# Kernel tuning notes

Hardware: AMD Instinct MI355X
Metric: run time of the kernel (lower is better)

The kernel has to match this reference:

```python
import jax, jax.numpy as jnp
import numpy as np

N = 100000
E = 1600000
IN_CH, HID_CH, OUT_CH, HEADS = 128, 32, 64, 4
NEG_SLOPE = 0.2


def gat_conv(x, src, dst, W, att_src, att_dst, bias, concat):
    """PyG-style GATConv (inference; dropout off). src/dst include self-loops.
    x: [N, Fin], W: [Fin, H*C], att_*: [H, C], bias: [H*C] or [C]."""
    n = x.shape[0]
    H, C = att_src.shape
    h = (x @ W).reshape(n, H, C)                      # [N, H, C]
    a_s = jnp.sum(h * att_src, axis=-1)               # [N, H]
    a_d = jnp.sum(h * att_dst, axis=-1)               # [N, H]
    e = jax.nn.leaky_relu(a_s[src] + a_d[dst], NEG_SLOPE)   # [E, H]
    # segment softmax over incoming edges of each dst node
    e_max = jax.ops.segment_max(e, dst, num_segments=n)     # [N, H]
    e_exp = jnp.exp(e - e_max[dst])                          # [E, H]
    denom = jax.ops.segment_sum(e_exp, dst, num_segments=n) # [N, H]
    alpha = e_exp / (denom[dst] + 1e-16)                     # [E, H]
    msg = h[src] * alpha[:, :, None]                         # [E, H, C]
    out = jax.ops.segment_sum(msg, dst, num_segments=n)     # [N, H, C]
    out = out.reshape(n, H * C) if concat else out.mean(axis=1)
    return out + bias


def setup_inputs() -> dict:
    key = jax.random.key(0)
    ks = jax.random.split(key, 10)
    g = 1.0 / np.sqrt(IN_CH)
    g2 = 1.0 / np.sqrt(HID_CH * HEADS)
    return {
        "x": jax.random.normal(ks[0], (N, IN_CH), dtype=jnp.float32),
        "edge_index": jax.random.randint(ks[1], (2, E), 0, N, dtype=jnp.int64),
        "W1": jax.random.normal(ks[2], (IN_CH, HEADS * HID_CH), dtype=jnp.float32) * g,
        "att_src1": jax.random.normal(ks[3], (HEADS, HID_CH), dtype=jnp.float32) * g,
        "att_dst1": jax.random.normal(ks[4], (HEADS, HID_CH), dtype=jnp.float32) * g,
        "b1": jnp.zeros((HEADS * HID_CH,), dtype=jnp.float32),
        "W2": jax.random.normal(ks[5], (HEADS * HID_CH, OUT_CH), dtype=jnp.float32) * g2,
        "att_src2": jax.random.normal(ks[6], (1, OUT_CH), dtype=jnp.float32) * g2,
        "att_dst2": jax.random.normal(ks[7], (1, OUT_CH), dtype=jnp.float32) * g2,
        "b2": jnp.zeros((OUT_CH,), dtype=jnp.float32),
    }


def reference(x, edge_index, W1, att_src1, att_dst1, b1, W2, att_src2, att_dst2, b2):
    n = x.shape[0]
    # GATConv adds self-loops by default (fixed-size concat: jit friendly)
    loops = jnp.arange(n, dtype=edge_index.dtype)
    src = jnp.concatenate([edge_index[0], loops])
    dst = jnp.concatenate([edge_index[1], loops])
    h = gat_conv(x, src, dst, W1, att_src1, att_dst1, b1, concat=True)
    h = jax.nn.elu(h)
    return gat_conv(h, src, dst, W2, att_src2, att_dst2, b2, concat=False)
```

## Files before the change

kernel.cpp:

```cpp
#include <hip/hip_runtime.h>
#include <hip/hip_fp16.h>

#define NEG_SLOPE 0.2f
#define BKN 128
#define MAXNB 1024
#define GRP 256

typedef _Float16 half_t;
typedef __attribute__((ext_vector_type(4))) _Float16 half4;
typedef __attribute__((ext_vector_type(8))) _Float16 half8;
typedef __attribute__((ext_vector_type(4))) float floatx4;

__device__ __forceinline__ float4 h4_to_f4(half4 h) {
    return make_float4((float)h[0], (float)h[1], (float)h[2], (float)h[3]);
}

__global__ __launch_bounds__(256) void w_convert2(
    const float* __restrict__ W1, half_t* __restrict__ Wt1,
    const float* __restrict__ W2, half_t* __restrict__ Wt2)
{
    int i = blockIdx.x * 256 + threadIdx.x;
    if (i < 128 * 128) {
        int k = i / 128, nn = i % 128;
        Wt1[nn * 128 + k] = (half_t)W1[i];
    } else if (i < 128 * 128 + 128 * 64) {
        int j = i - 128 * 128;
        int k = j / 64, nn = j % 64;
        Wt2[nn * 128 + k] = (half_t)W2[j];
    }
}

template<int BN, int HEADS>
__global__ __launch_bounds__(256) void gemm_mfma(
    const float* __restrict__ X, const half_t* __restrict__ Wt,
    const float* __restrict__ atts, const float* __restrict__ attd,
    half_t* __restrict__ H, float* __restrict__ As, float* __restrict__ Ad,
    int n)
{
    constexpr int K  = 128;
    constexpr int NT = BN / 16;
    constexpr int TPH = NT / HEADS;

    __shared__ half_t Wl[BN * K];
    __shared__ half_t Xl[64 * K];

    const int t = threadIdx.x;
    const int wave = t >> 6, lane = t & 63;
    const int quad = lane >> 4, c = lane & 15;

    float att_s[NT], att_d[NT];
    #pragma unroll
    for (int nt = 0; nt < NT; ++nt) {
        att_s[nt] = atts[nt * 16 + c];
        att_d[nt] = attd[nt * 16 + c];
    }

    for (int i = t; i < BN * 16; i += 256) {
        int row = i >> 4, cid = i & 15;
        half8 v = *(const half8*)(Wt + row * K + cid * 8);
        *(half8*)(Wl + row * K + ((cid ^ (row & 15)) << 3)) = v;
    }

    const int numTiles = (n + 63) / 64;
    for (int tile = blockIdx.x; tile < numTiles; tile += gridDim.x) {
        const int row0 = tile * 64;
        __syncthreads();
        for (int i = t; i < 1024; i += 256) {
            int m = i >> 4, cid = i & 15;
            int row = row0 + m;
            float4 a = make_float4(0.f,0.f,0.f,0.f), b = a;
            if (row < n) {
                const float4* src = (const float4*)(X + (size_t)row * K + cid * 8);
                a = src[0]; b = src[1];
            }
            half8 h;
            h[0]=(half_t)a.x; h[1]=(half_t)a.y; h[2]=(half_t)a.z; h[3]=(half_t)a.w;
            h[4]=(half_t)b.x; h[5]=(half_t)b.y; h[6]=(half_t)b.z; h[7]=(half_t)b.w;
            *(half8*)(Xl + m * K + ((cid ^ (m & 15)) << 3)) = h;
        }
        __syncthreads();

        floatx4 acc[NT];
        #pragma unroll
        for (int i = 0; i < NT; ++i) acc[i] = (floatx4)(0.f);

        #pragma unroll
        for (int kc = 0; kc < 4; ++kc) {
            int cid = kc * 4 + quad;
            half8 afrag = *(const half8*)(Xl + (wave * 16 + c) * K + ((cid ^ c) << 3));
            #pragma unroll
            for (int nt = 0; nt < NT; ++nt) {
                half8 bfrag = *(const half8*)(Wl + (nt * 16 + c) * K + ((cid ^ c) << 3));
                acc[nt] = __builtin_amdgcn_mfma_f32_16x16x32_f16(afrag, bfrag, acc[nt], 0, 0, 0);
            }
        }

        #pragma unroll
        for (int reg = 0; reg < 4; ++reg) {
            int row = row0 + wave * 16 + quad * 4 + reg;
            bool ok = row < n;
            if (ok) {
                #pragma unroll
                for (int nt = 0; nt < NT; ++nt)
                    H[(size_t)row * BN + nt * 16 + c] = (half_t)acc[nt][reg];
            }
            #pragma unroll
            for (int h = 0; h < HEADS; ++h) {
                float ps = 0.f, pd = 0.f;
                #pragma unroll
                for (int u = 0; u < TPH; ++u) {
                    int nt = h * TPH + u;
                    ps += acc[nt][reg] * att_s[nt];
                    pd += acc[nt][reg] * att_d[nt];
                }
                #pragma unroll
                for (int off = 1; off < 16; off <<= 1) {
                    ps += __shfl_xor(ps, off);
                    pd += __shfl_xor(pd, off);
                }
                if (ok && c == 0) {
                    As[(size_t)row * HEADS + h] = ps;
                    Ad[(size_t)row * HEADS + h] = pd;
                }
            }
        }
    }
}

__global__ __launch_bounds__(256) void ghist(
    const int* __restrict__ ei, int E, int Etot, int NB, int chunk,
    int* __restrict__ cnt)
{
    __shared__ int h[MAXNB];
    int g = blockIdx.x;
    for (int i = threadIdx.x; i < NB; i += 256) h[i] = 0;
    __syncthreads();
    int lo = g * chunk, hi = min(Etot, lo + chunk);
    for (int e = lo + threadIdx.x; e < hi; e += 256) {
        int dst = (e < E) ? ei[E + e] : (e - E);
        atomicAdd(&h[dst >> 7], 1);
    }
    __syncthreads();
    for (int i = threadIdx.x; i < NB; i += 256) cnt[i * GRP + g] = h[i];
}

__global__ __launch_bounds__(256) void scan_blocks(
    int* __restrict__ data, int n, int* __restrict__ bsum)
{
    __shared__ int s[256];
    int t = threadIdx.x;
    int idx = blockIdx.x * 1024 + t * 4;
    int4 v = make_int4(0, 0, 0, 0);
    if (idx + 3 < n)      v = *(const int4*)(data + idx);
    else {
        if (idx     < n) v.x = data[idx];
        if (idx + 1 < n) v.y = data[idx+1];
        if (idx + 2 < n) v.z = data[idx+2];
        if (idx + 3 < n) v.w = data[idx+3];
    }
    int tsum = v.x + v.y + v.z + v.w;
    s[t] = tsum;
    __syncthreads();
    for (int off = 1; off < 256; off <<= 1) {
        int x = (t >= off) ? s[t - off] : 0;
        __syncthreads();
        s[t] += x;
        __syncthreads();
    }
    int excl = s[t] - tsum;
    if (t == 255) bsum[blockIdx.x] = s[255];
    if (idx     < n) data[idx]     = excl;
    if (idx + 1 < n) data[idx + 1] = excl + v.x;
    if (idx + 2 < n) data[idx + 2] = excl + v.x + v.y;
    if (idx + 3 < n) data[idx + 3] = excl + v.x + v.y + v.z;
}

__global__ __launch_bounds__(256) void scan_sums(int* __restrict__ bsum, int nb)
{
    __shared__ int s[256];
    int t = threadIdx.x;
    int v = (t < nb) ? bsum[t] : 0;
    s[t] = v;
    __syncthreads();
    for (int off = 1; off < 256; off <<= 1) {
        int x = (t >= off) ? s[t - off] : 0;
        __syncthreads();
        s[t] += x;
        __syncthreads();
    }
    if (t < nb) bsum[t] = s[t] - v;
}

__global__ __launch_bounds__(256) void scan_add(
    int* __restrict__ data, int n, const int* __restrict__ bsum)
{
    int i = blockIdx.x * 256 + threadIdx.x;
    if (i < n) data[i] += bsum[i >> 10];
}

__global__ __launch_bounds__(256) void pass1_scatter(
    const int* __restrict__ ei, int E, int Etot, int NB, int chunk,
    const int* __restrict__ S, unsigned* __restrict__ tmp)
{
    __shared__ int cur[MAXNB];
    int g = blockIdx.x;
    for (int i = threadIdx.x; i < NB; i += 256) cur[i] = S[i * GRP + g];
    __syncthreads();
    int lo = g * chunk, hi = min(Etot, lo + chunk);
    for (int e = lo + threadIdx.x; e < hi; e += 256) {
        int src, dst;
        if (e < E) { src = ei[e]; dst = ei[E + e]; }
        else       { src = dst = e - E; }
        int pos = atomicAdd(&cur[dst >> 7], 1);
        tmp[pos] = ((unsigned)src << 7) | (unsigned)(dst & (BKN - 1));
    }
}

__global__ __launch_bounds__(256) void pass2_sort(
    const unsigned* __restrict__ tmp, const int* __restrict__ S,
    int NB, int Etot,
    int* __restrict__ offs, int* __restrict__ esrc, int n)
{
    __shared__ int cnt[BKN];
    __shared__ int sc[BKN];
    __shared__ int cur[BKN];
    int bk = blockIdx.x;
    int t  = threadIdx.x;
    if (t < BKN) cnt[t] = 0;
    __syncthreads();
    int lo = S[bk * GRP];
    int hi = (bk + 1 < NB) ? S[(bk + 1) * GRP] : Etot;
    for (int i = lo + t; i < hi; i += 256)
        atomicAdd(&cnt[tmp[i] & (BKN - 1)], 1);
    __syncthreads();
    int v = (t < BKN) ? cnt[t] : 0;
    if (t < BKN) sc[t] = v;
    __syncthreads();
    for (int off = 1; off < BKN; off <<= 1) {
        int x = (t < BKN && t >= off) ? sc[t - off] : 0;
        __syncthreads();
        if (t < BKN) sc[t] += x;
        __syncthreads();
    }
    if (t < BKN) {
        int node = bk * BKN + t;
        if (node < n) offs[node] = lo + sc[t];
        cur[t] = lo + sc[t] - v;
    }
    __syncthreads();
    for (int i = lo + t; i < hi; i += 256) {
        unsigned w = tmp[i];
        int p = atomicAdd(&cur[w & (BKN - 1)], 1);
        esrc[p] = (int)(w >> 7);
    }
}

__global__ __launch_bounds__(256) void agg1(
    const int* __restrict__ offs, const int* __restrict__ esrc,
    const half4* __restrict__ H4, const float* __restrict__ As,
    const float* __restrict__ Ad, const float* __restrict__ bias,
    float* __restrict__ X2, int n)
{
    int v    = (blockIdx.x * 256 + threadIdx.x) >> 6;
    int lane = threadIdx.x & 63;
    if (v >= n) return;
    int half = lane >> 5;
    int li   = lane & 31;
    int head = li >> 3;
    int end = offs[v];
    int beg = v ? offs[v - 1] : 0;
    float adv = Ad[(size_t)v * 4 + head];
    float a0 = 0.f, a1 = 0.f, a2 = 0.f, a3 = 0.f, den = 0.f;
    int j = beg + half;
    for (; j + 3 < end; j += 4) {
        int s0 = esrc[j], s1 = esrc[j + 2];
        float e0 = As[(size_t)s0 * 4 + head] + adv;
        float e1 = As[(size_t)s1 * 4 + head] + adv;
        half4 q0 = H4[(unsigned)s0 * 32 + li];
        half4 q1 = H4[(unsigned)s1 * 32 + li];
        e0 = e0 > 0.f ? e0 : NEG_SLOPE * e0;  float w0 = __expf(e0);
        e1 = e1 > 0.f ? e1 : NEG_SLOPE * e1;  float w1 = __expf(e1);
        float4 f0 = h4_to_f4(q0);
        float4 f1 = h4_to_f4(q1);
        a0 += w0 * f0.x + w1 * f1.x;
        a1 += w0 * f0.y + w1 * f1.y;
        a2 += w0 * f0.z + w1 * f1.z;
        a3 += w0 * f0.w + w1 * f1.w;
        den += w0 + w1;
    }
    for (; j < end; j += 2) {
        int s = esrc[j];
        float e = As[(size_t)s * 4 + head] + adv;
        e = e > 0.f ? e : NEG_SLOPE * e;
        float w = __expf(e);
        float4 f = h4_to_f4(H4[(unsigned)s * 32 + li]);
        a0 += w * f.x; a1 += w * f.y; a2 += w * f.z; a3 += w * f.w;
        den += w;
    }
    a0 += __shfl_xor(a0, 32);
    a1 += __shfl_xor(a1, 32);
    a2 += __shfl_xor(a2, 32);
    a3 += __shfl_xor(a3, 32);
    den += __shfl_xor(den, 32);
    if (half == 0) {
        float inv = 1.f / (den + 1e-16f);
        float4 b = ((const float4*)bias)[li];
        float o0 = a0 * inv + b.x, o1 = a1 * inv + b.y;
        float o2 = a2 * inv + b.z, o3 = a3 * inv + b.w;
        o0 = o0 > 0.f ? o0 : __expf(o0) - 1.f;
        o1 = o1 > 0.f ? o1 : __expf(o1) - 1.f;
        o2 = o2 > 0.f ? o2 : __expf(o2) - 1.f;
        o3 = o3 > 0.f ? o3 : __expf(o3) - 1.f;
        ((float4*)(X2 + (size_t)v * 128))[li] = make_float4(o0, o1, o2, o3);
    }
}

__global__ __launch_bounds__(256) void agg2(
    const int* __restrict__ offs, const int* __restrict__ esrc,
    const half4* __restrict__ H4, const float* __restrict__ As,
    const float* __restrict__ Ad, const float* __restrict__ bias,
    float* __restrict__ out, int n)
{
    int v    = (blockIdx.x * 256 + threadIdx.x) >> 6;
    int lane = threadIdx.x & 63;
    if (v >= n) return;
    int q  = lane >> 4;
    int li = lane & 15;
    int end = offs[v];
    int beg = v ? offs[v - 1] : 0;
    float adv = Ad[v];
    float a0 = 0.f, a1 = 0.f, a2 = 0.f, a3 = 0.f, den = 0.f;
    int j = beg + q;
    for (; j + 7 < end; j += 8) {
        int s0 = esrc[j], s1 = esrc[j + 4];
        float e0 = As[s0] + adv;
        float e1 = As[s1] + adv;
        half4 q0 = H4[(unsigned)s0 * 16 + li];
        half4 q1 = H4[(unsigned)s1 * 16 + li];
        e0 = e0 > 0.f ? e0 : NEG_SLOPE * e0;  float w0 = __expf(e0);
        e1 = e1 > 0.f ? e1 : NEG_SLOPE * e1;  float w1 = __expf(e1);
        float4 f0 = h4_to_f4(q0);
        float4 f1 = h4_to_f4(q1);
        a0 += w0 * f0.x + w1 * f1.x;
        a1 += w0 * f0.y + w1 * f1.y;
        a2 += w0 * f0.z + w1 * f1.z;
        a3 += w0 * f0.w + w1 * f1.w;
        den += w0 + w1;
    }
    for (; j < end; j += 4) {
        int s = esrc[j];
        float e = As[s] + adv;
        e = e > 0.f ? e : NEG_SLOPE * e;
        float w = __expf(e);
        float4 f = h4_to_f4(H4[(unsigned)s * 16 + li]);
        a0 += w * f.x; a1 += w * f.y; a2 += w * f.z; a3 += w * f.w;
        den += w;
    }
    #pragma unroll
    for (int off = 16; off <= 32; off <<= 1) {
        a0 += __shfl_xor(a0, off);
        a1 += __shfl_xor(a1, off);
        a2 += __shfl_xor(a2, off);
        a3 += __shfl_xor(a3, off);
        den += __shfl_xor(den, off);
    }
    if (lane < 16) {
        float inv = 1.f / (den + 1e-16f);
        float4 b = ((const float4*)bias)[li];
        ((float4*)(out + (size_t)v * 64))[li] =
            make_float4(a0 * inv + b.x, a1 * inv + b.y,
                        a2 * inv + b.z, a3 * inv + b.w);
    }
}

extern "C" void kernel_launch(void* const* d_in, const int* in_sizes, int n_in,
                              void* d_out, int out_size, void* d_ws, size_t ws_size,
                              hipStream_t stream)
{
    (void)n_in; (void)out_size; (void)ws_size;
    const float* x   = (const float*)d_in[0];
    const int*   ei  = (const int*)  d_in[1];
    const float* W1  = (const float*)d_in[2];
    const float* as1 = (const float*)d_in[3];
    const float* ad1 = (const float*)d_in[4];
    const float* b1  = (const float*)d_in[5];
    const float* W2  = (const float*)d_in[6];
    const float* as2 = (const float*)d_in[7];
    const float* ad2 = (const float*)d_in[8];
    const float* b2  = (const float*)d_in[9];
    float* out = (float*)d_out;

    const int n    = in_sizes[0] / 128;
    const int E    = in_sizes[1] / 2;
    const int Etot = E + n;
    const int NB   = (n + BKN - 1) / BKN;
    const int chunk = (Etot + GRP - 1) / GRP;

    char* p = (char*)d_ws;
    half_t* Hh = (half_t*)p;  p += (size_t)n * 128 * sizeof(half_t);
    float* X2  = (float*)p;   p += (size_t)n * 128 * sizeof(float);
    float* As1 = (float*)p;   p += (size_t)n * 4 * sizeof(float);
    float* Ad1 = (float*)p;   p += (size_t)n * 4 * sizeof(float);
    int* offs  = (int*)p;     p += (size_t)n * sizeof(int);
    int* esrc  = (int*)p;     p += (size_t)Etot * sizeof(int);
    unsigned* tmp = (unsigned*)p; p += (size_t)Etot * sizeof(unsigned);
    int* cnt   = (int*)p;     p += (size_t)NB * GRP * sizeof(int);
    int* bsum  = (int*)p;     p += 1024;
    half_t* Wt1 = (half_t*)p; p += 128 * 128 * sizeof(half_t);
    half_t* Wt2 = (half_t*)p; p += 64 * 128 * sizeof(half_t);

    const int scan_n  = NB * GRP;
    const int scan_nb = (scan_n + 1023) / 1024;

    w_convert2<<<(128 * 192 + 255) / 256, 256, 0, stream>>>(W1, Wt1, W2, Wt2);

    ghist<<<GRP, 256, 0, stream>>>(ei, E, Etot, NB, chunk, cnt);
    scan_blocks<<<scan_nb, 256, 0, stream>>>(cnt, scan_n, bsum);
    scan_sums<<<1, 256, 0, stream>>>(bsum, scan_nb);
    scan_add<<<(scan_n + 255) / 256, 256, 0, stream>>>(cnt, scan_n, bsum);
    pass1_scatter<<<GRP, 256, 0, stream>>>(ei, E, Etot, NB, chunk, cnt, tmp);
    pass2_sort<<<NB, 256, 0, stream>>>(tmp, cnt, NB, Etot, offs, esrc, n);

    const int gtiles = (n + 63) / 64;

    gemm_mfma<128, 4><<<gtiles, 256, 0, stream>>>(x, Wt1, as1, ad1, Hh, As1, Ad1, n);
    agg1<<<(n * 64 + 255) / 256, 256, 0, stream>>>(offs, esrc, (const half4*)Hh, As1, Ad1, b1, X2, n);

    gemm_mfma<64, 1><<<gtiles, 256, 0, stream>>>(X2, Wt2, as2, ad2, Hh, As1, Ad1, n);
    agg2<<<(n * 64 + 255) / 256, 256, 0, stream>>>(offs, esrc, (const half4*)Hh, As1, Ad1, b2, out, n);
}
```

Measured before the change: 344.3 us.

## Store layer-1 output in fp16 and widen aggregation gathers to half8

The layer-1 aggregation now writes its ELU output as fp16 instead of fp32, and the second GEMM reads half inputs directly through a new template flag. This halves the intermediate write and read traffic. Both aggregation kernels switch from half4 to half8 gathers per lane, so more edges are processed in parallel per wavefront (4 and 8 edge groups instead of 2 and 4). The cost is extra shuffle reductions, more accumulator registers, and a small precision loss from rounding the intermediate activations to fp16.

```diff
diff --git a/kernel.cpp b/kernel.cpp
--- a/kernel.cpp
+++ b/kernel.cpp
@@ -10,10 +10,6 @@
 typedef __attribute__((ext_vector_type(4))) _Float16 half4;
 typedef __attribute__((ext_vector_type(8))) _Float16 half8;
 typedef __attribute__((ext_vector_type(4))) float floatx4;
-
-__device__ __forceinline__ float4 h4_to_f4(half4 h) {
-    return make_float4((float)h[0], (float)h[1], (float)h[2], (float)h[3]);
-}
 
 __global__ __launch_bounds__(256) void w_convert2(
     const float* __restrict__ W1, half_t* __restrict__ Wt1,
@@ -30,9 +26,9 @@
     }
 }
 
-template<int BN, int HEADS>
+template<int BN, int HEADS, bool INHALF>
 __global__ __launch_bounds__(256) void gemm_mfma(
-    const float* __restrict__ X, const half_t* __restrict__ Wt,
+    const void* __restrict__ Xv, const half_t* __restrict__ Wt,
     const float* __restrict__ atts, const float* __restrict__ attd,
     half_t* __restrict__ H, float* __restrict__ As, float* __restrict__ Ad,
     int n)
@@ -68,14 +64,19 @@
         for (int i = t; i < 1024; i += 256) {
             int m = i >> 4, cid = i & 15;
             int row = row0 + m;
-            float4 a = make_float4(0.f,0.f,0.f,0.f), b = a;
+            half8 h;
+            #pragma unroll
+            for (int z = 0; z < 8; ++z) h[z] = (half_t)0.f;
             if (row < n) {
-                const float4* src = (const float4*)(X + (size_t)row * K + cid * 8);
-                a = src[0]; b = src[1];
+                if constexpr (INHALF) {
+                    h = *(const half8*)((const half_t*)Xv + (size_t)row * K + cid * 8);
+                } else {
+                    const float4* src = (const float4*)((const float*)Xv + (size_t)row * K + cid * 8);
+                    float4 a = src[0], b = src[1];
+                    h[0]=(half_t)a.x; h[1]=(half_t)a.y; h[2]=(half_t)a.z; h[3]=(half_t)a.w;
+                    h[4]=(half_t)b.x; h[5]=(half_t)b.y; h[6]=(half_t)b.z; h[7]=(half_t)b.w;
+                }
             }
-            half8 h;
-            h[0]=(half_t)a.x; h[1]=(half_t)a.y; h[2]=(half_t)a.z; h[3]=(half_t)a.w;
-            h[4]=(half_t)b.x; h[5]=(half_t)b.y; h[6]=(half_t)b.z; h[7]=(half_t)b.w;
             *(half8*)(Xl + m * K + ((cid ^ (m & 15)) << 3)) = h;
         }
         __syncthreads();
@@ -257,119 +258,133 @@
 
 __global__ __launch_bounds__(256) void agg1(
     const int* __restrict__ offs, const int* __restrict__ esrc,
-    const half4* __restrict__ H4, const float* __restrict__ As,
+    const half8* __restrict__ H8, const float* __restrict__ As,
     const float* __restrict__ Ad, const float* __restrict__ bias,
-    float* __restrict__ X2, int n)
+    half_t* __restrict__ X2h, int n)
 {
     int v    = (blockIdx.x * 256 + threadIdx.x) >> 6;
     int lane = threadIdx.x & 63;
     if (v >= n) return;
-    int half = lane >> 5;
-    int li   = lane & 31;
-    int head = li >> 3;
+    int q    = lane >> 4;
+    int li   = lane & 15;
+    int head = li >> 2;
     int end = offs[v];
     int beg = v ? offs[v - 1] : 0;
     float adv = Ad[(size_t)v * 4 + head];
-    float a0 = 0.f, a1 = 0.f, a2 = 0.f, a3 = 0.f, den = 0.f;
-    int j = beg + half;
-    for (; j + 3 < end; j += 4) {
-        int s0 = esrc[j], s1 = esrc[j + 2];
+    float a[8];
+    #pragma unroll
+    for (int f = 0; f < 8; ++f) a[f] = 0.f;
+    float den = 0.f;
+    int j = beg + q;
+    for (; j + 4 < end; j += 8) {
+        int s0 = esrc[j], s1 = esrc[j + 4];
         float e0 = As[(size_t)s0 * 4 + head] + adv;
         float e1 = As[(size_t)s1 * 4 + head] + adv;
-        half4 q0 = H4[(unsigned)s0 * 32 + li];
-        half4 q1 = H4[(unsigned)s1 * 32 + li];
+        half8 q0 = H8[(unsigned)s0 * 16 + li];
+        half8 q1 = H8[(unsigned)s1 * 16 + li];
         e0 = e0 > 0.f ? e0 : NEG_SLOPE * e0;  float w0 = __expf(e0);
         e1 = e1 > 0.f ? e1 : NEG_SLOPE * e1;  float w1 = __expf(e1);
-        float4 f0 = h4_to_f4(q0);
-        float4 f1 = h4_to_f4(q1);
-        a0 += w0 * f0.x + w1 * f1.x;
-        a1 += w0 * f0.y + w1 * f1.y;
-        a2 += w0 * f0.z + w1 * f1.z;
-        a3 += w0 * f0.w + w1 * f1.w;
+        #pragma unroll
+        for (int f = 0; f < 8; ++f)
+            a[f] += w0 * (float)q0[f] + w1 * (float)q1[f];
         den += w0 + w1;
     }
-    for (; j < end; j += 2) {
+    for (; j < end; j += 4) {
         int s = esrc[j];
         float e = As[(size_t)s * 4 + head] + adv;
+        half8 q0 = H8[(unsigned)s * 16 + li];
         e = e > 0.f ? e : NEG_SLOPE * e;
         float w = __expf(e);
-        float4 f = h4_to_f4(H4[(unsigned)s * 32 + li]);
-        a0 += w * f.x; a1 += w * f.y; a2 += w * f.z; a3 += w * f.w;
+        #pragma unroll
+        for (int f = 0; f < 8; ++f) a[f] += w * (float)q0[f];
         den += w;
     }
-    a0 += __shfl_xor(a0, 32);
-    a1 += __shfl_xor(a1, 32);
-    a2 += __shfl_xor(a2, 32);
-    a3 += __shfl_xor(a3, 32);
+    #pragma unroll
+    for (int f = 0; f < 8; ++f) {
+        a[f] += __shfl_xor(a[f], 16);
+        a[f] += __shfl_xor(a[f], 32);
+    }
+    den += __shfl_xor(den, 16);
     den += __shfl_xor(den, 32);
-    if (half == 0) {
+    if (q == 0) {
         float inv = 1.f / (den + 1e-16f);
-        float4 b = ((const float4*)bias)[li];
-        float o0 = a0 * inv + b.x, o1 = a1 * inv + b.y;
-        float o2 = a2 * inv + b.z, o3 = a3 * inv + b.w;
-        o0 = o0 > 0.f ? o0 : __expf(o0) - 1.f;
-        o1 = o1 > 0.f ? o1 : __expf(o1) - 1.f;
-        o2 = o2 > 0.f ? o2 : __expf(o2) - 1.f;
-        o3 = o3 > 0.f ? o3 : __expf(o3) - 1.f;
-        ((float4*)(X2 + (size_t)v * 128))[li] = make_float4(o0, o1, o2, o3);
+        float4 b0 = ((const float4*)bias)[2 * li];
+        float4 b1 = ((const float4*)bias)[2 * li + 1];
+        float o[8];
+        o[0] = a[0] * inv + b0.x; o[1] = a[1] * inv + b0.y;
+        o[2] = a[2] * inv + b0.z; o[3] = a[3] * inv + b0.w;
+        o[4] = a[4] * inv + b1.x; o[5] = a[5] * inv + b1.y;
+        o[6] = a[6] * inv + b1.z; o[7] = a[7] * inv + b1.w;
+        half8 h;
+        #pragma unroll
+        for (int f = 0; f < 8; ++f) {
+            float e = o[f] > 0.f ? o[f] : __expf(o[f]) - 1.f;
+            h[f] = (half_t)e;
+        }
+        *(half8*)(X2h + (size_t)v * 128 + li * 8) = h;
     }
 }
 
 __global__ __launch_bounds__(256) void agg2(
     const int* __restrict__ offs, const int* __restrict__ esrc,
-    const half4* __restrict__ H4, const float* __restrict__ As,
+    const half8* __restrict__ H8, const float* __restrict__ As,
     const float* __restrict__ Ad, const float* __restrict__ bias,
     float* __restrict__ out, int n)
 {
     int v    = (blockIdx.x * 256 + threadIdx.x) >> 6;
     int lane = threadIdx.x & 63;
     if (v >= n) return;
-    int q  = lane >> 4;
-    int li = lane & 15;
+    int g  = lane >> 3;
+    int li = lane & 7;
     int end = offs[v];
     int beg = v ? offs[v - 1] : 0;
     float adv = Ad[v];
-    float a0 = 0.f, a1 = 0.f, a2 = 0.f, a3 = 0.f, den = 0.f;
-    int j = beg + q;
-    for (; j + 7 < end; j += 8) {
-        int s0 = esrc[j], s1 = esrc[j + 4];
+    float a[8];
+    #pragma unroll
+    for (int f = 0; f < 8; ++f) a[f] = 0.f;
+    float den = 0.f;
+    int j = beg + g;
+    for (; j + 8 < end; j += 16) {
+        int s0 = esrc[j], s1 = esrc[j + 8];
         float e0 = As[s0] + adv;
         float e1 = As[s1] + adv;
-        half4 q0 = H4[(unsigned)s0 * 16 + li];
-        half4 q1 = H4[(unsigned)s1 * 16 + li];
+        half8 q0 = H8[(unsigned)s0 * 8 + li];
+        half8 q1 = H8[(unsigned)s1 * 8 + li];
         e0 = e0 > 0.f ? e0 : NEG_SLOPE * e0;  float w0 = __expf(e0);
         e1 = e1 > 0.f ? e1 : NEG_SLOPE * e1;  float w1 = __expf(e1);
-        float4 f0 = h4_to_f4(q0);
-        float4 f1 = h4_to_f4(q1);
-        a0 += w0 * f0.x + w1 * f1.x;
-        a1 += w0 * f0.y + w1 * f1.y;
-        a2 += w0 * f0.z + w1 * f1.z;
-        a3 += w0 * f0.w + w1 * f1.w;
+        #pragma unroll
+        for (int f = 0; f < 8; ++f)
+            a[f] += w0 * (float)q0[f] + w1 * (float)q1[f];
         den += w0 + w1;
     }
-    for (; j < end; j += 4) {
+    for (; j < end; j += 8) {
         int s = esrc[j];
         float e = As[s] + adv;
+        half8 q0 = H8[(unsigned)s * 8 + li];
         e = e > 0.f ? e : NEG_SLOPE * e;
         float w = __expf(e);
-        float4 f = h4_to_f4(H4[(unsigned)s * 16 + li]);
-        a0 += w * f.x; a1 += w * f.y; a2 += w * f.z; a3 += w * f.w;
+        #pragma unroll
+        for (int f = 0; f < 8; ++f) a[f] += w * (float)q0[f];
         den += w;
     }
     #pragma unroll
-    for (int off = 16; off <= 32; off <<= 1) {
-        a0 += __shfl_xor(a0, off);
-        a1 += __shfl_xor(a1, off);
-        a2 += __shfl_xor(a2, off);
-        a3 += __shfl_xor(a3, off);
-        den += __shfl_xor(den, off);
-    }
-    if (lane < 16) {
+    for (int f = 0; f < 8; ++f) {
+        a[f] += __shfl_xor(a[f], 8);
+        a[f] += __shfl_xor(a[f], 16);
+        a[f] += __shfl_xor(a[f], 32);
+    }
+    den += __shfl_xor(den, 8);
+    den += __shfl_xor(den, 16);
+    den += __shfl_xor(den, 32);
+    if (lane < 8) {
         float inv = 1.f / (den + 1e-16f);
-        float4 b = ((const float4*)bias)[li];
-        ((float4*)(out + (size_t)v * 64))[li] =
-            make_float4(a0 * inv + b.x, a1 * inv + b.y,
-                        a2 * inv + b.z, a3 * inv + b.w);
+        float4 b0 = ((const float4*)bias)[2 * li];
+        float4 b1 = ((const float4*)bias)[2 * li + 1];
+        float4* o4 = (float4*)(out + (size_t)v * 64);
+        o4[2 * li]     = make_float4(a[0] * inv + b0.x, a[1] * inv + b0.y,
+                                     a[2] * inv + b0.z, a[3] * inv + b0.w);
+        o4[2 * li + 1] = make_float4(a[4] * inv + b1.x, a[5] * inv + b1.y,
+                                     a[6] * inv + b1.z, a[7] * inv + b1.w);
     }
 }
 
@@ -397,8 +412,8 @@
     const int chunk = (Etot + GRP - 1) / GRP;
 
     char* p = (char*)d_ws;
-    half_t* Hh = (half_t*)p;  p += (size_t)n * 128 * sizeof(half_t);
-    float* X2  = (float*)p;   p += (size_t)n * 128 * sizeof(float);
+    half_t* Hh  = (half_t*)p; p += (size_t)n * 128 * sizeof(half_t);
+    half_t* X2h = (half_t*)p; p += (size_t)n * 128 * sizeof(half_t);
     float* As1 = (float*)p;   p += (size_t)n * 4 * sizeof(float);
     float* Ad1 = (float*)p;   p += (size_t)n * 4 * sizeof(float);
     int* offs  = (int*)p;     p += (size_t)n * sizeof(int);
@@ -423,9 +438,9 @@
 
     const int gtiles = (n + 63) / 64;
 
-    gemm_mfma<128, 4><<<gtiles, 256, 0, stream>>>(x, Wt1, as1, ad1, Hh, As1, Ad1, n);
-    agg1<<<(n * 64 + 255) / 256, 256, 0, stream>>>(offs, esrc, (const half4*)Hh, As1, Ad1, b1, X2, n);
-
-    gemm_mfma<64, 1><<<gtiles, 256, 0, stream>>>(X2, Wt2, as2, ad2, Hh, As1, Ad1, n);
-    agg2<<<(n * 64 + 255) / 256, 256, 0, stream>>>(offs, esrc, (const half4*)Hh, As1, Ad1, b2, out, n);
-}
+    gemm_mfma<128, 4, false><<<gtiles, 256, 0, stream>>>(x, Wt1, as1, ad1, Hh, As1, Ad1, n);
+    agg1<<<(n * 64 + 255) / 256, 256, 0, stream>>>(offs, esrc, (const half8*)Hh, As1, Ad1, b1, X2h, n);
+
+    gemm_mfma<64, 1, true><<<gtiles, 256, 0, stream>>>(X2h, Wt2, as2, ad2, Hh, As1, Ad1, n);
+    agg2<<<(n * 64 + 255) / 256, 256, 0, stream>>>(offs, esrc, (const half8*)Hh, As1, Ad1, b2, out, n);
+}
```

Measured after the change: 322.4 us. -6.4%, faster.
